# Performance work log

Hardware: AMD Instinct MI355X
Metric: run time of the kernel (lower is better)

The kernel has to match this reference:

```python
import jax, jax.numpy as jnp
import numpy as np

BETA = 0.5
IGNORE_INDEX = -100
N_ROWS = 4096
VOCAB = 32000


def setup_inputs() -> dict:
    key = jax.random.key(0)
    k1, k2, k3 = jax.random.split(key, 3)
    log_q = jax.random.normal(k1, (N_ROWS, VOCAB), dtype=jnp.float32)
    log_p = jax.random.normal(k2, (N_ROWS, VOCAB), dtype=jnp.float32)
    label = jax.random.randint(k3, (N_ROWS,), 0, VOCAB, dtype=jnp.int64)
    return {"log_q": log_q, "log_p": log_p, "label": label}


def reference(log_q, log_p, label):
    log_p = log_p.astype(jnp.float32).reshape(-1, log_p.shape[-1])
    log_q = log_q.astype(jnp.float32).reshape(-1, log_q.shape[-1])
    p = jnp.exp(log_p)
    q = jnp.exp(log_q)
    # m = lerp(q, p, beta) = (1-beta)*q + beta*p
    m = q + BETA * (p - q)
    log_m = jnp.log(m)
    # KLDivLoss(log_target=True)(input, target) = exp(target) * (target - input)
    kl_p = jnp.sum(p * (log_p - log_m), axis=-1)  # [N]
    kl_q = jnp.sum(q * (log_q - log_m), axis=-1)  # [N]
    loss = BETA * kl_p + (1.0 - BETA) * kl_q
    mask = label != IGNORE_INDEX
    loss = jnp.where(mask, loss, 0.0)
    n = jnp.sum(mask).astype(jnp.float32)
    total = jnp.where(n > 0, jnp.sum(loss) / jnp.maximum(n, 1.0), 0.0)
    return total.astype(jnp.float32)
```

## Files before the change

### kernel.cpp

```cpp
#include <hip/hip_runtime.h>

#define VOCAB 32000
#define NROWS 4096
#define IGNORE_INDEX (-100)

__global__ __launch_bounds__(256) void jsd_rows_kernel(
    const float* __restrict__ log_q,
    const float* __restrict__ log_p,
    const int* __restrict__ label,
    float* __restrict__ row_loss) {
  const int row = blockIdx.x;
  const float4* lp4 = reinterpret_cast<const float4*>(log_p) + (size_t)row * (VOCAB / 4);
  const float4* lq4 = reinterpret_cast<const float4*>(log_q) + (size_t)row * (VOCAB / 4);

  float acc = 0.0f;
  for (int i = threadIdx.x; i < VOCAB / 4; i += 256) {
    float4 lp = lp4[i];
    float4 lq = lq4[i];
    const float* lpc = reinterpret_cast<const float*>(&lp);
    const float* lqc = reinterpret_cast<const float*>(&lq);
#pragma unroll
    for (int c = 0; c < 4; ++c) {
      float lpv = lpc[c];
      float lqv = lqc[c];
      float p = __expf(lpv);
      float q = __expf(lqv);
      float m = 0.5f * (p + q);
      float lm = __logf(m);
      acc += p * (lpv - lm) + q * (lqv - lm);
    }
  }

#pragma unroll
  for (int off = 32; off > 0; off >>= 1) acc += __shfl_down(acc, off, 64);

  __shared__ float smem[4];
  const int lane = threadIdx.x & 63;
  const int wid = threadIdx.x >> 6;
  if (lane == 0) smem[wid] = acc;
  __syncthreads();
  if (threadIdx.x == 0) {
    float total = smem[0] + smem[1] + smem[2] + smem[3];
    bool valid = (label[row] != IGNORE_INDEX);
    row_loss[row] = valid ? 0.5f * total : 0.0f;
  }
}

__global__ __launch_bounds__(256) void jsd_finalize_kernel(
    const float* __restrict__ row_loss,
    const int* __restrict__ label,
    float* __restrict__ out) {
  float sum = 0.0f;
  int cnt = 0;
  for (int i = threadIdx.x; i < NROWS; i += 256) {
    sum += row_loss[i];
    cnt += (label[i] != IGNORE_INDEX) ? 1 : 0;
  }
#pragma unroll
  for (int off = 32; off > 0; off >>= 1) {
    sum += __shfl_down(sum, off, 64);
    cnt += __shfl_down(cnt, off, 64);
  }
  __shared__ float ssum[4];
  __shared__ int scnt[4];
  const int lane = threadIdx.x & 63;
  const int wid = threadIdx.x >> 6;
  if (lane == 0) { ssum[wid] = sum; scnt[wid] = cnt; }
  __syncthreads();
  if (threadIdx.x == 0) {
    float total = ssum[0] + ssum[1] + ssum[2] + ssum[3];
    int n = scnt[0] + scnt[1] + scnt[2] + scnt[3];
    out[0] = (n > 0) ? total / fmaxf((float)n, 1.0f) : 0.0f;
  }
}

extern "C" void kernel_launch(void* const* d_in, const int* in_sizes, int n_in,
                              void* d_out, int out_size, void* d_ws, size_t ws_size,
                              hipStream_t stream) {
  const float* log_q = (const float*)d_in[0];
  const float* log_p = (const float*)d_in[1];
  const int* label = (const int*)d_in[2];
  float* out = (float*)d_out;
  float* row_loss = (float*)d_ws;

  jsd_rows_kernel<<<NROWS, 256, 0, stream>>>(log_q, log_p, label, row_loss);
  jsd_finalize_kernel<<<1, 256, 0, stream>>>(row_loss, label, out);
}
```

Baseline: 192.4 us.

## Fuse finalize into row kernel via last-block atomic ticket and nontemporal loads

Merges the separate finalize kernel into the row kernel: each block increments an atomic counter after writing its row loss, and the last block to finish performs the global reduction. The main loop gets a compile-time trip count with a separate tail, unroll by 2, and nontemporal vector loads for the streaming inputs. This removes one kernel launch and its gap but adds a memset launch, fences and an atomic per block.

After: 367.8 us. 1.91x slower.

```diff
diff --git a/kernel.cpp b/kernel.cpp
--- a/kernel.cpp
+++ b/kernel.cpp
@@ -3,86 +3,101 @@
 #define VOCAB 32000
 #define NROWS 4096
 #define IGNORE_INDEX (-100)
+#define TPB 256
+#define NITEMS (VOCAB / 4)
+#define FULL_ITERS (NITEMS / TPB)
+#define TAIL_BASE (FULL_ITERS * TPB)
 
-__global__ __launch_bounds__(256) void jsd_rows_kernel(
-    const float* __restrict__ log_q,
-    const float* __restrict__ log_p,
+typedef float f32x4 __attribute__((ext_vector_type(4)));
+
+__device__ __forceinline__ float jsd_term(float lpv, float lqv) {
+  float p = __expf(lpv);
+  float q = __expf(lqv);
+  float lm = __logf(0.5f * (p + q));
+  return p * (lpv - lm) + q * (lqv - lm);
+}
+
+__global__ __launch_bounds__(TPB) void jsd_fused_kernel(
+    const f32x4* __restrict__ lq4g,
+    const f32x4* __restrict__ lp4g,
     const int* __restrict__ label,
-    float* __restrict__ row_loss) {
+    float* __restrict__ row_loss,
+    unsigned int* __restrict__ counter,
+    float* __restrict__ out) {
   const int row = blockIdx.x;
-  const float4* lp4 = reinterpret_cast<const float4*>(log_p) + (size_t)row * (VOCAB / 4);
-  const float4* lq4 = reinterpret_cast<const float4*>(log_q) + (size_t)row * (VOCAB / 4);
+  const f32x4* lp4 = lp4g + (size_t)row * NITEMS;
+  const f32x4* lq4 = lq4g + (size_t)row * NITEMS;
 
   float acc = 0.0f;
-  for (int i = threadIdx.x; i < VOCAB / 4; i += 256) {
-    float4 lp = lp4[i];
-    float4 lq = lq4[i];
-    const float* lpc = reinterpret_cast<const float*>(&lp);
-    const float* lqc = reinterpret_cast<const float*>(&lq);
+#pragma unroll 2
+  for (int k = 0; k < FULL_ITERS; ++k) {
+    const int i = threadIdx.x + k * TPB;
+    f32x4 lp = __builtin_nontemporal_load(lp4 + i);
+    f32x4 lq = __builtin_nontemporal_load(lq4 + i);
 #pragma unroll
-    for (int c = 0; c < 4; ++c) {
-      float lpv = lpc[c];
-      float lqv = lqc[c];
-      float p = __expf(lpv);
-      float q = __expf(lqv);
-      float m = 0.5f * (p + q);
-      float lm = __logf(m);
-      acc += p * (lpv - lm) + q * (lqv - lm);
-    }
+    for (int c = 0; c < 4; ++c) acc += jsd_term(lp[c], lq[c]);
+  }
+  if (threadIdx.x < (NITEMS - TAIL_BASE)) {
+    const int i = TAIL_BASE + threadIdx.x;
+    f32x4 lp = __builtin_nontemporal_load(lp4 + i);
+    f32x4 lq = __builtin_nontemporal_load(lq4 + i);
+#pragma unroll
+    for (int c = 0; c < 4; ++c) acc += jsd_term(lp[c], lq[c]);
   }
 
 #pragma unroll
   for (int off = 32; off > 0; off >>= 1) acc += __shfl_down(acc, off, 64);
 
   __shared__ float smem[4];
+  __shared__ unsigned int ticket;
   const int lane = threadIdx.x & 63;
   const int wid = threadIdx.x >> 6;
   if (lane == 0) smem[wid] = acc;
   __syncthreads();
   if (threadIdx.x == 0) {
     float total = smem[0] + smem[1] + smem[2] + smem[3];
-    bool valid = (label[row] != IGNORE_INDEX);
-    row_loss[row] = valid ? 0.5f * total : 0.0f;
+    row_loss[row] = (label[row] != IGNORE_INDEX) ? 0.5f * total : 0.0f;
+    __threadfence();
+    ticket = atomicAdd(counter, 1u);
   }
-}
+  __syncthreads();
 
-__global__ __launch_bounds__(256) void jsd_finalize_kernel(
-    const float* __restrict__ row_loss,
-    const int* __restrict__ label,
-    float* __restrict__ out) {
-  float sum = 0.0f;
-  int cnt = 0;
-  for (int i = threadIdx.x; i < NROWS; i += 256) {
-    sum += row_loss[i];
-    cnt += (label[i] != IGNORE_INDEX) ? 1 : 0;
-  }
+  if (ticket == NROWS - 1) {
+    __threadfence();
+    float sum = 0.0f;
+    int cnt = 0;
+    const volatile float* rl = row_loss;
+    for (int i = threadIdx.x; i < NROWS; i += TPB) {
+      sum += rl[i];
+      cnt += (label[i] != IGNORE_INDEX) ? 1 : 0;
+    }
 #pragma unroll
-  for (int off = 32; off > 0; off >>= 1) {
-    sum += __shfl_down(sum, off, 64);
-    cnt += __shfl_down(cnt, off, 64);
-  }
-  __shared__ float ssum[4];
-  __shared__ int scnt[4];
-  const int lane = threadIdx.x & 63;
-  const int wid = threadIdx.x >> 6;
-  if (lane == 0) { ssum[wid] = sum; scnt[wid] = cnt; }
-  __syncthreads();
-  if (threadIdx.x == 0) {
-    float total = ssum[0] + ssum[1] + ssum[2] + ssum[3];
-    int n = scnt[0] + scnt[1] + scnt[2] + scnt[3];
-    out[0] = (n > 0) ? total / fmaxf((float)n, 1.0f) : 0.0f;
+    for (int off = 32; off > 0; off >>= 1) {
+      sum += __shfl_down(sum, off, 64);
+      cnt += __shfl_down(cnt, off, 64);
+    }
+    __shared__ float ssum[4];
+    __shared__ int scnt[4];
+    if (lane == 0) { ssum[wid] = sum; scnt[wid] = cnt; }
+    __syncthreads();
+    if (threadIdx.x == 0) {
+      float total = ssum[0] + ssum[1] + ssum[2] + ssum[3];
+      int n = scnt[0] + scnt[1] + scnt[2] + scnt[3];
+      out[0] = (n > 0) ? total / fmaxf((float)n, 1.0f) : 0.0f;
+    }
   }
 }
 
 extern "C" void kernel_launch(void* const* d_in, const int* in_sizes, int n_in,
                               void* d_out, int out_size, void* d_ws, size_t ws_size,
                               hipStream_t stream) {
-  const float* log_q = (const float*)d_in[0];
-  const float* log_p = (const float*)d_in[1];
+  const f32x4* log_q = (const f32x4*)d_in[0];
+  const f32x4* log_p = (const f32x4*)d_in[1];
   const int* label = (const int*)d_in[2];
   float* out = (float*)d_out;
   float* row_loss = (float*)d_ws;
+  unsigned int* counter = (unsigned int*)((char*)d_ws + NROWS * sizeof(float));
 
-  jsd_rows_kernel<<<NROWS, 256, 0, stream>>>(log_q, log_p, label, row_loss);
-  jsd_finalize_kernel<<<1, 256, 0, stream>>>(row_loss, label, out);
+  hipMemsetAsync(counter, 0, sizeof(unsigned int), stream);
+  jsd_fused_kernel<<<NROWS, TPB, 0, stream>>>(log_q, log_p, label, row_loss, counter, out);
 }
```
